# Kernel optimization log

Hardware: AMD Instinct MI355X
Metric: run time of the kernel (lower is better)

Reference implementation:

```python
import jax, jax.numpy as jnp
import numpy as np

B_SZ, L, D_MODEL = 8, 200, 256
D_STATE, D_CONV, N_BANDS = 64, 4, 4
D_INNER = 2 * D_MODEL
DT_RANK = -(-D_MODEL // 16)  # ceil(d_model/16) = 16
EPS = 1e-12


def setup_inputs() -> dict:
    key = jax.random.key(0)
    ks = jax.random.split(key, 12)
    s = lambda k, shape, scale: jax.random.normal(k, shape, jnp.float32) * scale
    return {
        "x": s(ks[0], (B_SZ, L, D_MODEL), 1.0),
        "cos_phi": s(ks[1], (B_SZ, N_BANDS, L), 1.0),
        "sin_phi": s(ks[2], (B_SZ, N_BANDS, L), 1.0),
        "delta_mag": jax.random.uniform(ks[3], (B_SZ, N_BANDS, L), jnp.float32),
        "W_in": s(ks[4], (D_MODEL, 2 * D_INNER), D_MODEL ** -0.5),
        "conv_w": s(ks[5], (D_INNER, 1, D_CONV), 0.5),
        "conv_b": jnp.zeros((D_INNER,), jnp.float32),
        "W_x": s(ks[6], (D_INNER, DT_RANK + 2 * D_STATE), D_INNER ** -0.5),
        "W_dt": s(ks[7], (DT_RANK, D_INNER), DT_RANK ** -0.5),
        "b_dt": jnp.zeros((D_INNER,), jnp.float32),
        "A_log": jnp.log(jnp.tile(jnp.arange(1, D_STATE + 1, dtype=jnp.float32), (D_INNER, 1))),
        "D_skip": jnp.ones((D_INNER,), jnp.float32),
        "W_out": s(ks[8], (D_INNER, D_MODEL), D_INNER ** -0.5),
        "gamma": jnp.ones((D_MODEL,), jnp.float32),
        "beta": jnp.zeros((D_MODEL,), jnp.float32),
        "W_phase": s(ks[9], (2 * N_BANDS, D_STATE), (2 * N_BANDS) ** -0.5),
    }


def _selective_scan(u, dt, A, B_st, C_st):
    # u, dt: [B,L,Di]; A: [Di,N]; B_st, C_st: [B,L,N]
    dA = jnp.exp(jnp.einsum('bld,dn->bldn', dt, A))          # [B,L,Di,N]
    dBu = jnp.einsum('bld,bln->bldn', dt, B_st) * u[..., None]  # [B,L,Di,N]

    def step(h, inputs):
        dA_t, dBu_t, C_t = inputs
        h = dA_t * h + dBu_t                                  # [B,Di,N]
        y = jnp.einsum('bdn,bn->bd', h, C_t)                  # [B,Di]
        return h, y

    h0 = jnp.zeros((u.shape[0], u.shape[2], A.shape[1]), u.dtype)
    xs = (jnp.swapaxes(dA, 0, 1), jnp.swapaxes(dBu, 0, 1), jnp.swapaxes(C_st, 0, 1))
    _, ys = jax.lax.scan(step, h0, xs)                        # ys: [L,B,Di]
    return jnp.swapaxes(ys, 0, 1)


def reference(x, cos_phi, sin_phi, delta_mag, W_in, conv_w, conv_b, W_x, W_dt, b_dt,
              A_log, D_skip, W_out, gamma, beta, W_phase):
    residual = x
    xz = x @ W_in                                             # [B,L,2*Di]
    x_m, z = jnp.split(xz, 2, axis=-1)

    # causal depthwise conv1d: torch pads both sides with d_conv-1 then trims to L,
    # equivalent to left-pad (d_conv-1) + valid conv
    xc = jnp.swapaxes(x_m, 1, 2)                              # [B,Di,L]
    xc = jax.lax.conv_general_dilated(
        xc, conv_w, window_strides=(1,), padding=[(D_CONV - 1, 0)],
        dimension_numbers=('NCH', 'OIH', 'NCH'), feature_group_count=D_INNER)
    xc = xc + conv_b[None, :, None]
    x_m = jax.nn.silu(jnp.swapaxes(xc, 1, 2))                 # [B,L,Di]

    xp = x_m @ W_x
    dt_lr = xp[..., :DT_RANK]
    B_st = xp[..., DT_RANK:DT_RANK + D_STATE]
    C_st = xp[..., DT_RANK + D_STATE:]

    dt = jax.nn.softplus(dt_lr @ W_dt + b_dt)                 # [B,L,Di]
    dmm = jnp.mean(delta_mag, axis=1)[..., None]              # [B,L,1]
    dt = dt * (1.0 + jax.nn.softplus(dmm))

    phase_feats = jnp.swapaxes(jnp.concatenate([cos_phi, sin_phi], axis=1), 1, 2)  # [B,L,2*n_bands]
    C_st = C_st + phase_feats @ W_phase

    A = -jnp.exp(A_log)
    y = _selective_scan(x_m, dt, A, B_st, C_st)
    y = y + x_m * D_skip
    y = y * jax.nn.silu(z)
    out = y @ W_out + residual

    mu = jnp.mean(out, axis=-1, keepdims=True)
    var = jnp.mean((out - mu) ** 2, axis=-1, keepdims=True)
    return (out - mu) * jax.lax.rsqrt(var + EPS) * gamma + beta
```

## Files before the change

### kernel.cpp

```cpp
#include <hip/hip_runtime.h>
#include <hip/hip_bf16.h>

#define B_SZ 8
#define LSEQ 200
#define DMODEL 256
#define DINNER 512
#define DSTATE 64
#define DTRANK 16
#define ROWS (B_SZ * LSEQ)

using bf16x8 = __attribute__((ext_vector_type(8))) short;
using f32x4  = __attribute__((ext_vector_type(4))) float;

__device__ __forceinline__ float softplusf(float x) {
    return (x > 20.f) ? x : log1pf(__expf(x));
}
__device__ __forceinline__ float siluf(float x) {
    return x / (1.f + __expf(-x));
}
__device__ __forceinline__ unsigned short f2bf(float f) {
    union { float f; unsigned int u; } v; v.f = f;
    unsigned int r = v.u + 0x7FFF + ((v.u >> 16) & 1);
    return (unsigned short)(r >> 16);
}
__device__ __forceinline__ float bf2f(unsigned short u) {
    union { unsigned int i; float f; } v;
    v.i = ((unsigned int)u) << 16;
    return v.f;
}

template<int CTRL>
__device__ __forceinline__ float dpp_movf(float x) {
    union { float f; int i; } c, r;
    c.f = x;
    r.i = __builtin_amdgcn_update_dpp(0, c.i, CTRL, 0xF, 0xF, true);
    return r.f;
}

__global__ __launch_bounds__(256) void prep_w_k(
    const float* __restrict__ x, const float* __restrict__ W_in,
    const float* __restrict__ W_x, const float* __restrict__ W_out,
    unsigned short* __restrict__ x_hi,  unsigned short* __restrict__ x_lo,
    unsigned short* __restrict__ WiT_hi, unsigned short* __restrict__ WiT_lo,
    unsigned short* __restrict__ WxT_hi, unsigned short* __restrict__ WxT_lo,
    unsigned short* __restrict__ WoT_hi, unsigned short* __restrict__ WoT_lo)
{
    int idx = blockIdx.x * 256 + threadIdx.x;
    float v;
    unsigned short *dh, *dl;
    size_t di;
    if (idx < 409600) {
        v = x[idx]; dh = x_hi; dl = x_lo; di = idx;
    } else if (idx < 409600 + 262144) {
        int l = idx - 409600;
        int n = l >> 8, k = l & 255;
        v = W_in[(size_t)k * 1024 + n]; dh = WiT_hi; dl = WiT_lo; di = l;
    } else if (idx < 409600 + 262144 + 73728) {
        int l = idx - (409600 + 262144);
        int n = l >> 9, k = l & 511;
        v = W_x[(size_t)k * 144 + n]; dh = WxT_hi; dl = WxT_lo; di = l;
    } else if (idx < 409600 + 262144 + 73728 + 131072) {
        int l = idx - (409600 + 262144 + 73728);
        int n = l >> 9, k = l & 511;
        v = W_out[(size_t)k * 256 + n]; dh = WoT_hi; dl = WoT_lo; di = l;
    } else return;
    unsigned short h = f2bf(v);
    dh[di] = h;
    dl[di] = f2bf(v - bf2f(h));
}

__global__ __launch_bounds__(256) void gemm_mfma(
    const unsigned short* __restrict__ A_hi, const unsigned short* __restrict__ A_lo,
    const unsigned short* __restrict__ BT_hi, const unsigned short* __restrict__ BT_lo,
    float* __restrict__ C, int M, int N, int K, const float* __restrict__ resid)
{
    __shared__ unsigned short As_hi[64 * 40], As_lo[64 * 40];
    __shared__ unsigned short Bs_hi[64 * 40], Bs_lo[64 * 40];

    const int t    = threadIdx.x;
    const int m0   = blockIdx.y * 64;
    const int n0   = blockIdx.x * 64;
    const int lane = t & 63;
    const int w    = t >> 6;
    const int wm   = (w >> 1) * 32;
    const int wn   = (w & 1) * 32;
    const int fr   = lane & 15;
    const int fq   = lane >> 4;

    const int sr = t >> 2;
    const int sc = (t & 3) * 8;

    f32x4 acc[2][2] = {};

    const size_t a_off = (size_t)(m0 + sr) * K + sc;
    const int    brow  = n0 + sr;
    const size_t b_off = (size_t)brow * K + sc;
    const bool   bok   = brow < N;

    for (int k0 = 0; k0 < K; k0 += 32) {
        int4 ah = *(const int4*)(A_hi + a_off + k0);
        int4 al = *(const int4*)(A_lo + a_off + k0);
        int4 bh = make_int4(0, 0, 0, 0), bl = make_int4(0, 0, 0, 0);
        if (bok) {
            bh = *(const int4*)(BT_hi + b_off + k0);
            bl = *(const int4*)(BT_lo + b_off + k0);
        }
        __syncthreads();
        *(int4*)&As_hi[sr * 40 + sc] = ah;
        *(int4*)&As_lo[sr * 40 + sc] = al;
        *(int4*)&Bs_hi[sr * 40 + sc] = bh;
        *(int4*)&Bs_lo[sr * 40 + sc] = bl;
        __syncthreads();

        bf16x8 a_h[2], a_l[2], b_h[2], b_l[2];
#pragma unroll
        for (int mi = 0; mi < 2; mi++) {
            int row = wm + mi * 16 + fr;
            a_h[mi] = *(const bf16x8*)&As_hi[row * 40 + fq * 8];
            a_l[mi] = *(const bf16x8*)&As_lo[row * 40 + fq * 8];
        }
#pragma unroll
        for (int ni = 0; ni < 2; ni++) {
            int row = wn + ni * 16 + fr;
            b_h[ni] = *(const bf16x8*)&Bs_hi[row * 40 + fq * 8];
            b_l[ni] = *(const bf16x8*)&Bs_lo[row * 40 + fq * 8];
        }
#pragma unroll
        for (int mi = 0; mi < 2; mi++)
#pragma unroll
            for (int ni = 0; ni < 2; ni++) {
                acc[mi][ni] = __builtin_amdgcn_mfma_f32_16x16x32_bf16(a_h[mi], b_h[ni], acc[mi][ni], 0, 0, 0);
                acc[mi][ni] = __builtin_amdgcn_mfma_f32_16x16x32_bf16(a_h[mi], b_l[ni], acc[mi][ni], 0, 0, 0);
                acc[mi][ni] = __builtin_amdgcn_mfma_f32_16x16x32_bf16(a_l[mi], b_h[ni], acc[mi][ni], 0, 0, 0);
            }
    }

#pragma unroll
    for (int mi = 0; mi < 2; mi++)
#pragma unroll
        for (int ni = 0; ni < 2; ni++) {
            int col = n0 + wn + ni * 16 + fr;
            if (col < N) {
#pragma unroll
                for (int reg = 0; reg < 4; reg++) {
                    int row = m0 + wm + mi * 16 + fq * 4 + reg;
                    float v = acc[mi][ni][reg];
                    if (resid) v += resid[(size_t)row * N + col];
                    C[(size_t)row * N + col] = v;
                }
            }
        }
}

__global__ __launch_bounds__(256) void conv_silu_k(
    const float* __restrict__ xz, const float* __restrict__ conv_w,
    const float* __restrict__ conv_b, float* __restrict__ xm,
    unsigned short* __restrict__ xm_hi, unsigned short* __restrict__ xm_lo)
{
    int idx = blockIdx.x * 256 + threadIdx.x;
    int c = idx & 511;
    int r = idx >> 9;
    int l = r % LSEQ;

    float w0 = conv_w[c * 4 + 0];
    float w1 = conv_w[c * 4 + 1];
    float w2 = conv_w[c * 4 + 2];
    float w3 = conv_w[c * 4 + 3];

    const float* base = xz + (size_t)r * 1024 + c;
    float acc = conv_b[c];
    if (l >= 3) acc = fmaf(base[-3 * 1024], w0, acc);
    if (l >= 2) acc = fmaf(base[-2 * 1024], w1, acc);
    if (l >= 1) acc = fmaf(base[-1 * 1024], w2, acc);
    acc = fmaf(base[0], w3, acc);

    float s = siluf(acc);
    xm[idx] = s;
    unsigned short h = f2bf(s);
    xm_hi[idx] = h;
    xm_lo[idx] = f2bf(s - bf2f(h));
}

__global__ __launch_bounds__(256) void pack_bc_k(
    const float* __restrict__ cosp, const float* __restrict__ sinp,
    const float* __restrict__ W_phase, const float* __restrict__ xp,
    float* __restrict__ bcp)
{
    int idx = blockIdx.x * 256 + threadIdx.x;
    int n = idx & 63;
    int r = idx >> 6;
    int b = r / LSEQ, l = r % LSEQ;

    float acc = 0.f;
#pragma unroll
    for (int j = 0; j < 4; j++) {
        float cp = cosp[(b * 4 + j) * LSEQ + l];
        float sp = sinp[(b * 4 + j) * LSEQ + l];
        acc = fmaf(cp, W_phase[j * 64 + n], acc);
        acc = fmaf(sp, W_phase[(4 + j) * 64 + n], acc);
    }
    float Bv = xp[(size_t)r * 144 + 16 + n];
    float Cv = xp[(size_t)r * 144 + 80 + n] + acc;
    *(float2*)&bcp[(size_t)r * 128 + 2 * n] = make_float2(Bv, Cv);
}

__global__ __launch_bounds__(256) void dtprep_k(
    const float* __restrict__ xp, const float* __restrict__ W_dt,
    const float* __restrict__ b_dt, const float* __restrict__ dmag,
    const float* __restrict__ xm, float2* __restrict__ dtpackT)
{
    const int blk = blockIdx.x;
    const int b   = blk >> 5;
    const int d0  = ((blk >> 2) & 7) * 64;
    const int l0  = (blk & 3) * 50;

    __shared__ float xr[50 * 17];
    __shared__ float scl[50];
    __shared__ float wlds[16 * 64];
    __shared__ float bbl[64];

    const int t = threadIdx.x;

    for (int idx = t; idx < 50 * 16; idx += 256) {
        int l = idx >> 4, i = idx & 15;
        xr[l * 17 + i] = xp[(size_t)(b * LSEQ + l0 + l) * 144 + i];
    }
    for (int idx = t; idx < 16 * 64; idx += 256) {
        int i = idx >> 6, dd = idx & 63;
        wlds[idx] = W_dt[i * 512 + d0 + dd];
    }
    if (t < 64) bbl[t] = b_dt[d0 + t];
    if (t >= 64 && t < 64 + 50) {
        int l = t - 64;
        float dm = 0.f;
#pragma unroll
        for (int j = 0; j < 4; j++)
            dm += dmag[(b * 4 + j) * LSEQ + l0 + l];
        scl[l] = 1.f + softplusf(dm * 0.25f);
    }
    __syncthreads();

    const int dd = t >> 2;
    const int lj = t & 3;
    const int d  = d0 + dd;

    float wreg[16];
#pragma unroll
    for (int k = 0; k < 16; k++)
        wreg[k] = wlds[k * 64 + dd];
    const float bb = bbl[dd];

    float2*      orow = dtpackT + (size_t)(b * 512 + d) * LSEQ + l0;
    const float* xmb  = xm + (size_t)(b * LSEQ + l0) * 512 + d;

#pragma unroll 1
    for (int i = 0; i < 13; i++) {
        int l = lj + 4 * i;
        if (l < 50) {
            float acc = bb;
#pragma unroll
            for (int k = 0; k < 16; k++)
                acc = fmaf(xr[l * 17 + k], wreg[k], acc);
            float dtv = softplusf(acc) * scl[l];
            float u = xmb[(size_t)l * 512];
            orow[l] = make_float2(dtv, dtv * u);
        }
    }
}

__global__ __launch_bounds__(256, 4) void scan_k(
    const float2* __restrict__ dtpackT, const float* __restrict__ bcp,
    const float* __restrict__ xm, const float* __restrict__ xz,
    const float* __restrict__ A_log, const float* __restrict__ D_skip,
    unsigned short* __restrict__ yf_hi, unsigned short* __restrict__ yf_lo)
{
    int bid  = blockIdx.x;
    int swz  = (bid & 7) * 128 + (bid >> 3);
    int wv0  = swz * 4 + (threadIdx.x >> 6);
    int wv   = __builtin_amdgcn_readfirstlane(wv0);
    int lane = threadIdx.x & 63;
    int b = wv >> 9;
    int d = wv & 511;

    float A2 = -__expf(A_log[d * 64 + lane]) * 1.4426950408889634f;
    float Dd = D_skip[d];

    const float4* dtp4 = (const float4*)(dtpackT + (size_t)(b * 512 + d) * LSEQ);
    const float*  bcr = bcp + (size_t)b * LSEQ * 128 + 2 * lane;
    const float*  xmb = xm  + (size_t)b * LSEQ * 512 + d;
    const float*  xzb = xz  + (size_t)b * LSEQ * 1024 + 512 + d;
    unsigned short* yph = yf_hi + (size_t)b * LSEQ * 512 + d;
    unsigned short* ypl = yf_lo + (size_t)b * LSEQ * 512 + d;

    const bool lo32 = (lane & 32) == 0;
    const bool lo16 = (lane & 16) == 0;
    const bool lo8  = (lane & 8)  == 0;
    const bool store_lane = (lane & 7) == 0;
    const int  tsel = ((lane >> 5) & 1) * 4 + ((lane >> 3) & 1) * 2 + ((lane >> 4) & 1);

    float h = 0.f;

    float2 bcA[8], bcB[8];
    float4 dqA[4], dqB[4];
    float uA, zA, uB, zB;

#define PREF(BC, DQ, L0)                                        \
    _Pragma("unroll")                                           \
    for (int t = 0; t < 8; t++)                                 \
        BC[t] = *(const float2*)&bcr[((L0) + t) * 128];         \
    _Pragma("unroll")                                           \
    for (int j = 0; j < 4; j++)                                 \
        DQ[j] = dtp4[((L0) >> 1) + j];

#define UZ(U, Z, L0)                                            \
    {                                                           \
        U = 0.f; Z = 0.f;                                       \
        if (store_lane) {                                       \
            int lu = (L0) + tsel;                               \
            U = xmb[lu * 512];                                  \
            Z = xzb[lu * 1024];                                 \
        }                                                       \
    }

#define STEP(BC, DQ, U, Z, L0)                                  \
    {                                                           \
        float p[8];                                             \
        _Pragma("unroll")                                       \
        for (int t = 0; t < 8; t++) {                           \
            float dtv = ((t & 1) == 0) ? DQ[t >> 1].x : DQ[t >> 1].z; \
            float dtu = ((t & 1) == 0) ? DQ[t >> 1].y : DQ[t >> 1].w; \
            float e = __builtin_amdgcn_exp2f(dtv * A2);         \
            h = fmaf(e, h, dtu * BC[t].x);                      \
            p[t] = h * BC[t].y;                                 \
        }                                                       \
         \
        float q[4];                                             \
        _Pragma("unroll")                                       \
        for (int i = 0; i < 4; i++) {                           \
            float keep = lo32 ? p[i] : p[i + 4];                \
            float send = lo32 ? p[i + 4] : p[i];                \
            q[i] = keep + __shfl_xor(send, 32, 64);             \
        }                                                       \
         \
        float r2[2];                                            \
        _Pragma("unroll")                                       \
        for (int i = 0; i < 2; i++) {                           \
            float kp = lo8 ? q[i] : q[i + 2];                   \
            float sd = lo8 ? q[i + 2] : q[i];                   \
            r2[i] = kp + dpp_movf<0x128>(sd);                   \
        }                                                       \
                                   \
        float keepf = lo16 ? r2[0] : r2[1];                     \
        float sendf = lo16 ? r2[1] : r2[0];                     \
        float s = keepf + __shfl_xor(sendf, 16, 64);            \
         \
        s += dpp_movf<0x104>(s);                                \
        s += dpp_movf<0x102>(s);                                \
        s += dpp_movf<0x101>(s);                                \
        if (store_lane) {                                       \
            int lu = (L0) + tsel;                               \
            float yv = (s + (U) * Dd) * siluf(Z);               \
            unsigned short hh = f2bf(yv);                       \
            yph[lu * 512] = hh;                                 \
            ypl[lu * 512] = f2bf(yv - bf2f(hh));                \
        }                                                       \
    }

    PREF(bcA, dqA, 0);
    int l0 = 0;
#pragma unroll 1
    for (int it = 0; it < 12; it++) {
        UZ(uA, zA, l0);
        PREF(bcB, dqB, l0 + 8);
        STEP(bcA, dqA, uA, zA, l0);
        UZ(uB, zB, l0 + 8);
        PREF(bcA, dqA, l0 + 16);
        STEP(bcB, dqB, uB, zB, l0 + 8);
        l0 += 16;
    }
    UZ(uA, zA, 192);
    STEP(bcA, dqA, uA, zA, 192);

#undef PREF
#undef UZ
#undef STEP
}

__global__ __launch_bounds__(256) void ln_k(
    const float* __restrict__ outp, const float* __restrict__ gamma,
    const float* __restrict__ beta, float* __restrict__ out)
{
    int r = blockIdx.x;
    int t = threadIdx.x;
    float v = outp[(size_t)r * 256 + t];
    float s = v, ss = v * v;
#pragma unroll
    for (int off = 32; off > 0; off >>= 1) {
        s  += __shfl_xor(s,  off, 64);
        ss += __shfl_xor(ss, off, 64);
    }
    __shared__ float red[8];
    int w = t >> 6;
    if ((t & 63) == 0) { red[w] = s; red[4 + w] = ss; }
    __syncthreads();
    s  = red[0] + red[1] + red[2] + red[3];
    ss = red[4] + red[5] + red[6] + red[7];
    float mu  = s * (1.f / 256.f);
    float var = ss * (1.f / 256.f) - mu * mu;
    if (var < 0.f) var = 0.f;
    float inv = rsqrtf(var + 1e-12f);
    float o = (v - mu) * inv * gamma[t] + beta[t];
    out[(size_t)r * 256 + t] = o;
}

extern "C" void kernel_launch(void* const* d_in, const int* in_sizes, int n_in,
                              void* d_out, int out_size, void* d_ws, size_t ws_size,
                              hipStream_t stream)
{
    const float* x       = (const float*)d_in[0];
    const float* cosp    = (const float*)d_in[1];
    const float* sinp    = (const float*)d_in[2];
    const float* dmag    = (const float*)d_in[3];
    const float* W_in    = (const float*)d_in[4];
    const float* conv_w  = (const float*)d_in[5];
    const float* conv_b  = (const float*)d_in[6];
    const float* W_x     = (const float*)d_in[7];
    const float* W_dt    = (const float*)d_in[8];
    const float* b_dt    = (const float*)d_in[9];
    const float* A_log   = (const float*)d_in[10];
    const float* D_skip  = (const float*)d_in[11];
    const float* W_out   = (const float*)d_in[12];
    const float* gamma   = (const float*)d_in[13];
    const float* beta    = (const float*)d_in[14];
    const float* W_phase = (const float*)d_in[15];
    float* out = (float*)d_out;

    char* ws = (char*)d_ws;
    float*  xz     = (float*)ws;  ws += (size_t)ROWS * 1024 * 4;
    float*  xm     = (float*)ws;  ws += (size_t)ROWS * 512 * 4;
    float*  xp     = (float*)ws;  ws += (size_t)ROWS * 144 * 4;
    float*  bcp    = (float*)ws;  ws += (size_t)ROWS * 128 * 4;
    float2* dtpack = (float2*)ws; ws += (size_t)ROWS * 512 * 8;
    float*  outp   = (float*)ws;  ws += (size_t)ROWS * 256 * 4;
    unsigned short* x_hi   = (unsigned short*)ws; ws += (size_t)ROWS * 256 * 2;
    unsigned short* x_lo   = (unsigned short*)ws; ws += (size_t)ROWS * 256 * 2;
    unsigned short* WiT_hi = (unsigned short*)ws; ws += (size_t)1024 * 256 * 2;
    unsigned short* WiT_lo = (unsigned short*)ws; ws += (size_t)1024 * 256 * 2;
    unsigned short* WxT_hi = (unsigned short*)ws; ws += (size_t)144 * 512 * 2;
    unsigned short* WxT_lo = (unsigned short*)ws; ws += (size_t)144 * 512 * 2;
    unsigned short* WoT_hi = (unsigned short*)ws; ws += (size_t)256 * 512 * 2;
    unsigned short* WoT_lo = (unsigned short*)ws; ws += (size_t)256 * 512 * 2;
    unsigned short* xm_hi  = (unsigned short*)ws; ws += (size_t)ROWS * 512 * 2;
    unsigned short* xm_lo  = (unsigned short*)ws; ws += (size_t)ROWS * 512 * 2;
    unsigned short* yf_hi  = (unsigned short*)ws; ws += (size_t)ROWS * 512 * 2;
    unsigned short* yf_lo  = (unsigned short*)ws; ws += (size_t)ROWS * 512 * 2;

    dim3 blk(256);
    prep_w_k   <<<dim3(3424),   blk, 0, stream>>>(x, W_in, W_x, W_out,
                                                  x_hi, x_lo, WiT_hi, WiT_lo,
                                                  WxT_hi, WxT_lo, WoT_hi, WoT_lo);
    gemm_mfma  <<<dim3(16, 25), blk, 0, stream>>>(x_hi, x_lo, WiT_hi, WiT_lo,
                                                  xz, ROWS, 1024, 256, nullptr);
    conv_silu_k<<<dim3(3200),   blk, 0, stream>>>(xz, conv_w, conv_b, xm, xm_hi, xm_lo);
    gemm_mfma  <<<dim3(3, 25),  blk, 0, stream>>>(xm_hi, xm_lo, WxT_hi, WxT_lo,
                                                  xp, ROWS, 144, 512, nullptr);
    pack_bc_k  <<<dim3(400),    blk, 0, stream>>>(cosp, sinp, W_phase, xp, bcp);
    dtprep_k   <<<dim3(256),    blk, 0, stream>>>(xp, W_dt, b_dt, dmag, xm, dtpack);
    scan_k     <<<dim3(1024),   blk, 0, stream>>>(dtpack, bcp, xm, xz, A_log, D_skip,
                                                  yf_hi, yf_lo);
    gemm_mfma  <<<dim3(4, 25),  blk, 0, stream>>>(yf_hi, yf_lo, WoT_hi, WoT_lo,
                                                  outp, ROWS, 256, 512, x);
    ln_k       <<<dim3(1600),   blk, 0, stream>>>(outp, gamma, beta, out);
}
```

Measured before the change: 185.8 us.

## Fuse output GEMM with LayerNorm and merge B/C packing with dt prep

Adds a GEMM kernel whose 16-row tiles cover all 256 output columns, so the residual add and LayerNorm can run in its epilogue with an in-block row reduction. This removes the outp round trip and one launch. It also merges pack_bc_k and dtprep_k into a single launch that dispatches on block index. The trade-off is that the fused GEMM runs only 100 blocks with small A tiles, which lowers parallelism and reuse compared with the previous 4x25 tiled GEMM.

```diff
diff --git a/kernel.cpp b/kernel.cpp
--- a/kernel.cpp
+++ b/kernel.cpp
@@ -152,6 +152,115 @@
         }
 }
 
+__global__ __launch_bounds__(256) void gemm_ln_k(
+    const unsigned short* __restrict__ A_hi, const unsigned short* __restrict__ A_lo,
+    const unsigned short* __restrict__ BT_hi, const unsigned short* __restrict__ BT_lo,
+    const float* __restrict__ resid, const float* __restrict__ gamma,
+    const float* __restrict__ beta, float* __restrict__ out)
+{
+    __shared__ unsigned short As_hi[16 * 40], As_lo[16 * 40];
+    __shared__ unsigned short Bs_hi[256 * 40], Bs_lo[256 * 40];
+    __shared__ float rs[16][4], rss[16][4];
+
+    const int t    = threadIdx.x;
+    const int m0   = blockIdx.x * 16;
+    const int lane = t & 63;
+    const int w    = t >> 6;
+    const int fr   = lane & 15;
+    const int fq   = lane >> 4;
+    const int sr   = t >> 2;
+    const int sc   = (t & 3) * 8;
+
+    f32x4 acc[4] = {};
+
+    for (int k0 = 0; k0 < 512; k0 += 32) {
+        int4 ah, al;
+        const bool aok = t < 64;
+        if (aok) {
+            size_t a_off = (size_t)(m0 + (t >> 2)) * 512 + sc + k0;
+            ah = *(const int4*)(A_hi + a_off);
+            al = *(const int4*)(A_lo + a_off);
+        }
+        int4 bh[4], bl[4];
+#pragma unroll
+        for (int q = 0; q < 4; q++) {
+            size_t b_off = (size_t)(sr + q * 64) * 512 + sc + k0;
+            bh[q] = *(const int4*)(BT_hi + b_off);
+            bl[q] = *(const int4*)(BT_lo + b_off);
+        }
+        __syncthreads();
+        if (aok) {
+            *(int4*)&As_hi[(t >> 2) * 40 + sc] = ah;
+            *(int4*)&As_lo[(t >> 2) * 40 + sc] = al;
+        }
+#pragma unroll
+        for (int q = 0; q < 4; q++) {
+            *(int4*)&Bs_hi[(sr + q * 64) * 40 + sc] = bh[q];
+            *(int4*)&Bs_lo[(sr + q * 64) * 40 + sc] = bl[q];
+        }
+        __syncthreads();
+
+        bf16x8 a_h = *(const bf16x8*)&As_hi[fr * 40 + fq * 8];
+        bf16x8 a_l = *(const bf16x8*)&As_lo[fr * 40 + fq * 8];
+#pragma unroll
+        for (int ni = 0; ni < 4; ni++) {
+            int brow = w * 64 + ni * 16 + fr;
+            bf16x8 b_h = *(const bf16x8*)&Bs_hi[brow * 40 + fq * 8];
+            bf16x8 b_l = *(const bf16x8*)&Bs_lo[brow * 40 + fq * 8];
+            acc[ni] = __builtin_amdgcn_mfma_f32_16x16x32_bf16(a_h, b_h, acc[ni], 0, 0, 0);
+            acc[ni] = __builtin_amdgcn_mfma_f32_16x16x32_bf16(a_h, b_l, acc[ni], 0, 0, 0);
+            acc[ni] = __builtin_amdgcn_mfma_f32_16x16x32_bf16(a_l, b_h, acc[ni], 0, 0, 0);
+        }
+    }
+
+    float v[4][4];
+    float ps[4] = {}, pss[4] = {};
+#pragma unroll
+    for (int ni = 0; ni < 4; ni++) {
+        int col = w * 64 + ni * 16 + fr;
+#pragma unroll
+        for (int reg = 0; reg < 4; reg++) {
+            int row = m0 + fq * 4 + reg;
+            float val = acc[ni][reg] + resid[(size_t)row * 256 + col];
+            v[ni][reg] = val;
+            ps[reg] += val;
+            pss[reg] = fmaf(val, val, pss[reg]);
+        }
+    }
+#pragma unroll
+    for (int off = 1; off < 16; off <<= 1) {
+#pragma unroll
+        for (int reg = 0; reg < 4; reg++) {
+            ps[reg]  += __shfl_xor(ps[reg],  off, 64);
+            pss[reg] += __shfl_xor(pss[reg], off, 64);
+        }
+    }
+    if (fr == 0) {
+#pragma unroll
+        for (int reg = 0; reg < 4; reg++) {
+            rs[fq * 4 + reg][w]  = ps[reg];
+            rss[fq * 4 + reg][w] = pss[reg];
+        }
+    }
+    __syncthreads();
+#pragma unroll
+    for (int reg = 0; reg < 4; reg++) {
+        int r = fq * 4 + reg;
+        float s  = rs[r][0] + rs[r][1] + rs[r][2] + rs[r][3];
+        float ss = rss[r][0] + rss[r][1] + rss[r][2] + rss[r][3];
+        float mu  = s * (1.f / 256.f);
+        float var = ss * (1.f / 256.f) - mu * mu;
+        if (var < 0.f) var = 0.f;
+        float inv = rsqrtf(var + 1e-12f);
+#pragma unroll
+        for (int ni = 0; ni < 4; ni++) {
+            int col = w * 64 + ni * 16 + fr;
+            out[(size_t)(m0 + r) * 256 + col] =
+                (v[ni][reg] - mu) * inv * gamma[col] + beta[col];
+        }
+    }
+}
+
 __global__ __launch_bounds__(256) void conv_silu_k(
     const float* __restrict__ xz, const float* __restrict__ conv_w,
     const float* __restrict__ conv_b, float* __restrict__ xm,
@@ -181,45 +290,45 @@
     xm_lo[idx] = f2bf(s - bf2f(h));
 }
 
-__global__ __launch_bounds__(256) void pack_bc_k(
+__global__ __launch_bounds__(256) void pbdt_k(
     const float* __restrict__ cosp, const float* __restrict__ sinp,
     const float* __restrict__ W_phase, const float* __restrict__ xp,
-    float* __restrict__ bcp)
-{
-    int idx = blockIdx.x * 256 + threadIdx.x;
-    int n = idx & 63;
-    int r = idx >> 6;
-    int b = r / LSEQ, l = r % LSEQ;
-
-    float acc = 0.f;
-#pragma unroll
-    for (int j = 0; j < 4; j++) {
-        float cp = cosp[(b * 4 + j) * LSEQ + l];
-        float sp = sinp[(b * 4 + j) * LSEQ + l];
-        acc = fmaf(cp, W_phase[j * 64 + n], acc);
-        acc = fmaf(sp, W_phase[(4 + j) * 64 + n], acc);
-    }
-    float Bv = xp[(size_t)r * 144 + 16 + n];
-    float Cv = xp[(size_t)r * 144 + 80 + n] + acc;
-    *(float2*)&bcp[(size_t)r * 128 + 2 * n] = make_float2(Bv, Cv);
-}
-
-__global__ __launch_bounds__(256) void dtprep_k(
-    const float* __restrict__ xp, const float* __restrict__ W_dt,
-    const float* __restrict__ b_dt, const float* __restrict__ dmag,
-    const float* __restrict__ xm, float2* __restrict__ dtpackT)
-{
-    const int blk = blockIdx.x;
-    const int b   = blk >> 5;
-    const int d0  = ((blk >> 2) & 7) * 64;
-    const int l0  = (blk & 3) * 50;
-
+    float* __restrict__ bcp,
+    const float* __restrict__ W_dt, const float* __restrict__ b_dt,
+    const float* __restrict__ dmag, const float* __restrict__ xm,
+    float2* __restrict__ dtpackT)
+{
     __shared__ float xr[50 * 17];
     __shared__ float scl[50];
     __shared__ float wlds[16 * 64];
     __shared__ float bbl[64];
 
     const int t = threadIdx.x;
+
+    if (blockIdx.x < 400) {
+        int idx = blockIdx.x * 256 + t;
+        int n = idx & 63;
+        int r = idx >> 6;
+        int b = r / LSEQ, l = r % LSEQ;
+
+        float acc = 0.f;
+#pragma unroll
+        for (int j = 0; j < 4; j++) {
+            float cp = cosp[(b * 4 + j) * LSEQ + l];
+            float sp = sinp[(b * 4 + j) * LSEQ + l];
+            acc = fmaf(cp, W_phase[j * 64 + n], acc);
+            acc = fmaf(sp, W_phase[(4 + j) * 64 + n], acc);
+        }
+        float Bv = xp[(size_t)r * 144 + 16 + n];
+        float Cv = xp[(size_t)r * 144 + 80 + n] + acc;
+        *(float2*)&bcp[(size_t)r * 128 + 2 * n] = make_float2(Bv, Cv);
+        return;
+    }
+
+    const int blk = blockIdx.x - 400;
+    const int b   = blk >> 5;
+    const int d0  = ((blk >> 2) & 7) * 64;
+    const int l0  = (blk & 3) * 50;
 
     for (int idx = t; idx < 50 * 16; idx += 256) {
         int l = idx >> 4, i = idx & 15;
@@ -333,7 +442,6 @@
             h = fmaf(e, h, dtu * BC[t].x);                      \
             p[t] = h * BC[t].y;                                 \
         }                                                       \
-         \
         float q[4];                                             \
         _Pragma("unroll")                                       \
         for (int i = 0; i < 4; i++) {                           \
@@ -341,7 +449,6 @@
             float send = lo32 ? p[i + 4] : p[i];                \
             q[i] = keep + __shfl_xor(send, 32, 64);             \
         }                                                       \
-         \
         float r2[2];                                            \
         _Pragma("unroll")                                       \
         for (int i = 0; i < 2; i++) {                           \
@@ -349,11 +456,9 @@
             float sd = lo8 ? q[i + 2] : q[i];                   \
             r2[i] = kp + dpp_movf<0x128>(sd);                   \
         }                                                       \
-                                   \
         float keepf = lo16 ? r2[0] : r2[1];                     \
         float sendf = lo16 ? r2[1] : r2[0];                     \
         float s = keepf + __shfl_xor(sendf, 16, 64);            \
-         \
         s += dpp_movf<0x104>(s);                                \
         s += dpp_movf<0x102>(s);                                \
         s += dpp_movf<0x101>(s);                                \
@@ -384,33 +489,6 @@
 #undef PREF
 #undef UZ
 #undef STEP
-}
-
-__global__ __launch_bounds__(256) void ln_k(
-    const float* __restrict__ outp, const float* __restrict__ gamma,
-    const float* __restrict__ beta, float* __restrict__ out)
-{
-    int r = blockIdx.x;
-    int t = threadIdx.x;
-    float v = outp[(size_t)r * 256 + t];
-    float s = v, ss = v * v;
-#pragma unroll
-    for (int off = 32; off > 0; off >>= 1) {
-        s  += __shfl_xor(s,  off, 64);
-        ss += __shfl_xor(ss, off, 64);
-    }
-    __shared__ float red[8];
-    int w = t >> 6;
-    if ((t & 63) == 0) { red[w] = s; red[4 + w] = ss; }
-    __syncthreads();
-    s  = red[0] + red[1] + red[2] + red[3];
-    ss = red[4] + red[5] + red[6] + red[7];
-    float mu  = s * (1.f / 256.f);
-    float var = ss * (1.f / 256.f) - mu * mu;
-    if (var < 0.f) var = 0.f;
-    float inv = rsqrtf(var + 1e-12f);
-    float o = (v - mu) * inv * gamma[t] + beta[t];
-    out[(size_t)r * 256 + t] = o;
 }
 
 extern "C" void kernel_launch(void* const* d_in, const int* in_sizes, int n_in,
@@ -441,7 +519,6 @@
     float*  xp     = (float*)ws;  ws += (size_t)ROWS * 144 * 4;
     float*  bcp    = (float*)ws;  ws += (size_t)ROWS * 128 * 4;
     float2* dtpack = (float2*)ws; ws += (size_t)ROWS * 512 * 8;
-    float*  outp   = (float*)ws;  ws += (size_t)ROWS * 256 * 4;
     unsigned short* x_hi   = (unsigned short*)ws; ws += (size_t)ROWS * 256 * 2;
     unsigned short* x_lo   = (unsigned short*)ws; ws += (size_t)ROWS * 256 * 2;
     unsigned short* WiT_hi = (unsigned short*)ws; ws += (size_t)1024 * 256 * 2;
@@ -464,11 +541,10 @@
     conv_silu_k<<<dim3(3200),   blk, 0, stream>>>(xz, conv_w, conv_b, xm, xm_hi, xm_lo);
     gemm_mfma  <<<dim3(3, 25),  blk, 0, stream>>>(xm_hi, xm_lo, WxT_hi, WxT_lo,
                                                   xp, ROWS, 144, 512, nullptr);
-    pack_bc_k  <<<dim3(400),    blk, 0, stream>>>(cosp, sinp, W_phase, xp, bcp);
-    dtprep_k   <<<dim3(256),    blk, 0, stream>>>(xp, W_dt, b_dt, dmag, xm, dtpack);
+    pbdt_k     <<<dim3(656),    blk, 0, stream>>>(cosp, sinp, W_phase, xp, bcp,
+                                                  W_dt, b_dt, dmag, xm, dtpack);
     scan_k     <<<dim3(1024),   blk, 0, stream>>>(dtpack, bcp, xm, xz, A_log, D_skip,
                                                   yf_hi, yf_lo);
-    gemm_mfma  <<<dim3(4, 25),  blk, 0, stream>>>(yf_hi, yf_lo, WoT_hi, WoT_lo,
-                                                  outp, ROWS, 256, 512, x);
-    ln_k       <<<dim3(1600),   blk, 0, stream>>>(outp, gamma, beta, out);
-}
+    gemm_ln_k  <<<dim3(100),    blk, 0, stream>>>(yf_hi, yf_lo, WoT_hi, WoT_lo,
+                                                  x, gamma, beta, out);
+}
```

Measured after the change: 213.8 us. +15.1%, slower.
